# Kernel tuning notes

Measured on AMD Instinct MI355X. Metric: run time of the kernel, lower is better.

Reference implementation:

```python
import jax, jax.numpy as jnp
import numpy as np

N = 131072      # octree nodes at this depth
C_IN = 256      # in_channels == out_channels
C_B = 64        # bottleneck channels = out_channels // 4
K = 27          # 3x3x3 octree kernel neighborhood
EPS = 1e-5


def _bn(x, g, b, m, v):
    # inference-style BatchNorm with given running stats
    return (x - m) * (g * jax.lax.rsqrt(v + EPS)) + b


def setup_inputs() -> dict:
    key = jax.random.key(0)
    ks = jax.random.split(key, 20)
    inp = {
        "data": jax.random.normal(ks[0], (N, C_IN), dtype=jnp.float32),
        "neigh": jax.random.randint(ks[1], (N, K), 0, N, dtype=jnp.int32),
        "depth": 6,
        # conv1x1a (Linear, no bias) + BN
        "w1": jax.random.normal(ks[2], (C_IN, C_B), dtype=jnp.float32) * 0.05,
        "bn1_g": jax.random.uniform(ks[3], (C_B,), dtype=jnp.float32) + 0.5,
        "bn1_b": jax.random.normal(ks[4], (C_B,), dtype=jnp.float32) * 0.1,
        "bn1_m": jax.random.normal(ks[5], (C_B,), dtype=jnp.float32) * 0.1,
        "bn1_v": jax.random.uniform(ks[6], (C_B,), dtype=jnp.float32) + 0.5,
        # octree conv3x3 (27-neighbor gather + GEMM, no bias) + BN
        "w3": jax.random.normal(ks[7], (K, C_B, C_B), dtype=jnp.float32) * 0.02,
        "bn2_g": jax.random.uniform(ks[8], (C_B,), dtype=jnp.float32) + 0.5,
        "bn2_b": jax.random.normal(ks[9], (C_B,), dtype=jnp.float32) * 0.1,
        "bn2_m": jax.random.normal(ks[10], (C_B,), dtype=jnp.float32) * 0.1,
        "bn2_v": jax.random.uniform(ks[11], (C_B,), dtype=jnp.float32) + 0.5,
        # conv1x1b + BN (no ReLU)
        "w2": jax.random.normal(ks[12], (C_B, C_IN), dtype=jnp.float32) * 0.05,
        "bn3_g": jax.random.uniform(ks[13], (C_IN,), dtype=jnp.float32) + 0.5,
        "bn3_b": jax.random.normal(ks[14], (C_IN,), dtype=jnp.float32) * 0.1,
        "bn3_m": jax.random.normal(ks[15], (C_IN,), dtype=jnp.float32) * 0.1,
        "bn3_v": jax.random.uniform(ks[16], (C_IN,), dtype=jnp.float32) + 0.5,
    }
    return inp


def reference(data, neigh, depth, w1, bn1_g, bn1_b, bn1_m, bn1_v,
              w3, bn2_g, bn2_b, bn2_m, bn2_v,
              w2, bn3_g, bn3_b, bn3_m, bn3_v):
    # conv1x1a + BN + ReLU
    c1 = jax.nn.relu(_bn(data @ w1, bn1_g, bn1_b, bn1_m, bn1_v))  # [N, C_B]
    # octree conv3x3: gather 27 neighbors then contract with [K, C_B, C_B]
    gathered = c1[neigh]                                          # [N, K, C_B]
    c2 = jnp.einsum('nkc,kcd->nd', gathered, w3)                  # [N, C_B]
    c2 = jax.nn.relu(_bn(c2, bn2_g, bn2_b, bn2_m, bn2_v))
    # conv1x1b + BN (no relu)
    c3 = _bn(c2 @ w2, bn3_g, bn3_b, bn3_m, bn3_v)                 # [N, C_IN]
    # residual (in_channels == out_channels -> identity shortcut) + ReLU
    return jax.nn.relu(c3 + data)
```

## Files before the change

kernel.cpp:

```cpp
#include <hip/hip_runtime.h>

#define CIN 256
#define CB 64
#define KNB 27

typedef __attribute__((ext_vector_type(8))) short short8_t;
typedef __attribute__((ext_vector_type(4))) float f32x4;
typedef __attribute__((ext_vector_type(4))) int   i32x4;

__device__ inline unsigned short f2bf(float f) {
    union { float f; unsigned u; } x; x.f = f;
    unsigned r = x.u + 0x7fffu + ((x.u >> 16) & 1u);
    return (unsigned short)(r >> 16);
}
__device__ inline float bf2f(unsigned short h) {
    union { unsigned u; float f; } x; x.u = ((unsigned)h) << 16; return x.f;
}
__device__ inline f32x4 mfma16(short8_t a, short8_t b, f32x4 c) {
    return __builtin_amdgcn_mfma_f32_16x16x32_bf16(a, b, c, 0, 0, 0);
}
__device__ inline i32x4 mfma_i8(i32x4 a, i32x4 b, i32x4 c) {
    return __builtin_amdgcn_mfma_i32_16x16x64_i8(a, b, c, 0, 0, 0);
}

__global__ __launch_bounds__(64) void zero_kernel(unsigned* __restrict__ amax) {
    if (threadIdx.x < 4) amax[threadIdx.x] = 0u;
}

__global__ __launch_bounds__(256) void prep_a_kernel(
    const float* __restrict__ w1, const float* __restrict__ w2,
    const float* __restrict__ g1, const float* __restrict__ b1, const float* __restrict__ m1, const float* __restrict__ v1,
    const float* __restrict__ g2, const float* __restrict__ b2, const float* __restrict__ m2, const float* __restrict__ v2,
    const float* __restrict__ g3, const float* __restrict__ b3, const float* __restrict__ m3, const float* __restrict__ v3,
    unsigned short* __restrict__ w1p, unsigned short* __restrict__ w2p,
    float* __restrict__ bias1, float* __restrict__ bias2, float* __restrict__ bias3)
{
    int t = blockIdx.x * 256 + threadIdx.x;
    if (t < 16384) {
        int j = t & 7, lane = (t >> 3) & 63, tt = (t >> 9) & 3, s = t >> 11;
        int c = s * 32 + (lane >> 4) * 8 + j;
        int d = tt * 16 + (lane & 15);
        float sc = g1[d] * rsqrtf(v1[d] + 1e-5f);
        w1p[t] = f2bf(w1[c * CB + d] * sc);
    } else if (t < 32768) {
        int u = t - 16384;
        int j = u & 7, lane = (u >> 3) & 63, mt = (u >> 9) & 15, s = u >> 13;
        int c = s * 32 + (lane >> 4) * 8 + j;
        int d = mt * 16 + (lane & 15);
        float sc = g3[d] * rsqrtf(v3[d] + 1e-5f);
        w2p[u] = f2bf(w2[c * CIN + d] * sc);
    } else if (t < 33152) {
        int u = t - 32768;
        if (u < 64)       { float sc = g1[u] * rsqrtf(v1[u] + 1e-5f); bias1[u] = b1[u] - m1[u] * sc; }
        else if (u < 128) { int d = u - 64;  float sc = g2[d] * rsqrtf(v2[d] + 1e-5f); bias2[d] = b2[d] - m2[d] * sc; }
        else              { int d = u - 128; float sc = g3[d] * rsqrtf(v3[d] + 1e-5f); bias3[d] = b3[d] - m3[d] * sc; }
    }
}

__global__ __launch_bounds__(1024) void w3max_kernel(
    const float* __restrict__ w3, const float* __restrict__ g2, const float* __restrict__ v2,
    unsigned* __restrict__ amax)
{
    __shared__ float sm[16];
    int tid = threadIdx.x;
    float m = 0.f;
    for (int e = blockIdx.x * 1024 + tid; e < KNB * CB * CB; e += 8 * 1024) {
        int d = e & 63;
        float sc = g2[d] * rsqrtf(v2[d] + 1e-5f);
        m = fmaxf(m, fabsf(w3[e] * sc));
    }
#pragma unroll
    for (int off = 32; off; off >>= 1) m = fmaxf(m, __shfl_xor(m, off));
    if ((tid & 63) == 0) sm[tid >> 6] = m;
    __syncthreads();
    if (tid == 0) {
        float r = sm[0];
#pragma unroll
        for (int i = 1; i < 16; i++) r = fmaxf(r, sm[i]);
        atomicMax(&amax[1], __float_as_uint(r));
    }
}

__global__ __launch_bounds__(256) void prep_b_kernel(
    const float* __restrict__ w3, const float* __restrict__ g2, const float* __restrict__ v2,
    const unsigned* __restrict__ amax, signed char* __restrict__ w3q)
{
    int u = blockIdx.x * 256 + threadIdx.x;
    int j = u & 15, lane = (u >> 4) & 63, tile = (u >> 10) & 3, k = u >> 12;
    int c = (lane >> 4) * 16 + j;
    int d = tile * 16 + (lane & 15);
    float sw = __uint_as_float(amax[1]);
    float inv = sw > 0.f ? 127.f / sw : 0.f;
    float sc = g2[d] * rsqrtf(v2[d] + 1e-5f);
    int q = __float2int_rn(w3[(k * CB + c) * CB + d] * sc * inv);
    q = q > 127 ? 127 : (q < -127 ? -127 : q);
    w3q[u] = (signed char)q;
}

__global__ __launch_bounds__(256) void k1_conv1x1a(
    const float* __restrict__ data, const unsigned short* __restrict__ w1p,
    const float* __restrict__ bias1, unsigned short* __restrict__ c1b,
    float* __restrict__ blockmax)
{
    __shared__ short8_t w1s[2048];
    __shared__ float smax[4];
    int tid = threadIdx.x;
    const short8_t* wsrc = (const short8_t*)w1p;
#pragma unroll
    for (int i = 0; i < 8; i++) w1s[tid + i * 256] = wsrc[tid + i * 256];

    int lane = tid & 63, wave = tid >> 6;
    int g = lane >> 4, r = lane & 15;
    int rowbase = blockIdx.x * 128 + wave * 32;
    f32x4 acc[2][4] = {};
    __syncthreads();

#pragma unroll
    for (int s = 0; s < 8; s++) {
        short8_t a[2];
#pragma unroll
        for (int sub = 0; sub < 2; sub++) {
            const float* ap = data + (size_t)(rowbase + sub * 16 + r) * CIN + s * 32 + g * 8;
            float4 f0 = *(const float4*)ap;
            float4 f1 = *(const float4*)(ap + 4);
            short8_t av;
            av[0] = (short)f2bf(f0.x); av[1] = (short)f2bf(f0.y);
            av[2] = (short)f2bf(f0.z); av[3] = (short)f2bf(f0.w);
            av[4] = (short)f2bf(f1.x); av[5] = (short)f2bf(f1.y);
            av[6] = (short)f2bf(f1.z); av[7] = (short)f2bf(f1.w);
            a[sub] = av;
        }
#pragma unroll
        for (int t = 0; t < 4; t++) {
            short8_t b = w1s[(s * 4 + t) * 64 + lane];
            acc[0][t] = mfma16(a[0], b, acc[0][t]);
            acc[1][t] = mfma16(a[1], b, acc[1][t]);
        }
    }

    float mloc = 0.f;
#pragma unroll
    for (int sub = 0; sub < 2; sub++)
#pragma unroll
        for (int t = 0; t < 4; t++) {
            int col = t * 16 + r;
            float bs = bias1[col];
#pragma unroll
            for (int i = 0; i < 4; i++) {
                int row = rowbase + sub * 16 + g * 4 + i;
                float v = fmaxf(acc[sub][t][i] + bs, 0.f);
                mloc = fmaxf(mloc, v);
                c1b[row * CB + col] = f2bf(v);
            }
        }
#pragma unroll
    for (int off = 32; off; off >>= 1) mloc = fmaxf(mloc, __shfl_xor(mloc, off));
    if (lane == 0) smax[wave] = mloc;
    __syncthreads();
    if (tid == 0)
        blockmax[blockIdx.x] = fmaxf(fmaxf(smax[0], smax[1]), fmaxf(smax[2], smax[3]));
}

__global__ __launch_bounds__(1024) void c1max_kernel(
    const float* __restrict__ blockmax, unsigned* __restrict__ amax)
{
    __shared__ float sm[16];
    int tid = threadIdx.x;
    float m = blockmax[tid];
#pragma unroll
    for (int off = 32; off; off >>= 1) m = fmaxf(m, __shfl_xor(m, off));
    if ((tid & 63) == 0) sm[tid >> 6] = m;
    __syncthreads();
    if (tid == 0) {
        float r = sm[0];
#pragma unroll
        for (int i = 1; i < 16; i++) r = fmaxf(r, sm[i]);
        amax[0] = __float_as_uint(r);
    }
}

__global__ __launch_bounds__(256) void quant_c1_kernel(
    const unsigned short* __restrict__ c1b, const unsigned* __restrict__ amax,
    signed char* __restrict__ c1q)
{
    int t = blockIdx.x * 256 + threadIdx.x;
    float s1 = __uint_as_float(amax[0]);
    float inv = s1 > 0.f ? 127.f / s1 : 0.f;
    const short8_t* src = (const short8_t*)c1b;
    short8_t v0 = src[t * 2], v1 = src[t * 2 + 1];
    int ow[4];
#pragma unroll
    for (int h = 0; h < 4; h++) {
        int w = 0;
#pragma unroll
        for (int e = 0; e < 4; e++) {
            unsigned short hv = (unsigned short)((h < 2 ? v0 : v1)[(h & 1) * 4 + e]);
            int q = __float2int_rn(bf2f(hv) * inv);
            q = q > 127 ? 127 : q;
            w |= (q & 0xff) << (e * 8);
        }
        ow[h] = w;
    }
    ((int4*)c1q)[t] = make_int4(ow[0], ow[1], ow[2], ow[3]);
}

__global__ __launch_bounds__(64, 4) void k2_conv3x3(
    const signed char* __restrict__ c1q, const int* __restrict__ neigh,
    const signed char* __restrict__ w3q, const float* __restrict__ bias2,
    const unsigned* __restrict__ amax, unsigned short* __restrict__ c2b)
{
    __shared__ int nidx[32 * KNB];
    int tid = threadIdx.x;
    int rowbase = blockIdx.x * 32;

    const int4* nsrc = (const int4*)(neigh + (size_t)rowbase * KNB);
#pragma unroll
    for (int i = 0; i < 4; i++) {
        int p = tid + i * 64;
        if (p < 216) ((int4*)nidx)[p] = nsrc[p];
    }

    int lane = tid;
    int g = lane >> 4, r = lane & 15;
    float sf = __uint_as_float(amax[0]) * __uint_as_float(amax[1]) * (1.f / (127.f * 127.f));
    __syncthreads();

    const i32x4* bq = (const i32x4*)w3q;
    i32x4 iacc[2][4] = {};

#pragma unroll
    for (int k = 0; k < KNB; k++) {
        i32x4 b0 = bq[k * 256 + lane];
        i32x4 b1 = bq[k * 256 + 64 + lane];
        i32x4 b2 = bq[k * 256 + 128 + lane];
        i32x4 b3 = bq[k * 256 + 192 + lane];
        int i0 = nidx[r * KNB + k];
        int i1 = nidx[(16 + r) * KNB + k];
        i32x4 a0 = *(const i32x4*)(c1q + (size_t)i0 * CB + g * 16);
        i32x4 a1 = *(const i32x4*)(c1q + (size_t)i1 * CB + g * 16);
        iacc[0][0] = mfma_i8(a0, b0, iacc[0][0]);
        iacc[1][0] = mfma_i8(a1, b0, iacc[1][0]);
        iacc[0][1] = mfma_i8(a0, b1, iacc[0][1]);
        iacc[1][1] = mfma_i8(a1, b1, iacc[1][1]);
        iacc[0][2] = mfma_i8(a0, b2, iacc[0][2]);
        iacc[1][2] = mfma_i8(a1, b2, iacc[1][2]);
        iacc[0][3] = mfma_i8(a0, b3, iacc[0][3]);
        iacc[1][3] = mfma_i8(a1, b3, iacc[1][3]);
    }

#pragma unroll
    for (int sub = 0; sub < 2; sub++)
#pragma unroll
        for (int t = 0; t < 4; t++) {
            int col = t * 16 + r;
            float bs = bias2[col];
#pragma unroll
            for (int i = 0; i < 4; i++) {
                int row = rowbase + sub * 16 + g * 4 + i;
                float v = fmaxf((float)iacc[sub][t][i] * sf + bs, 0.f);
                c2b[row * CB + col] = f2bf(v);
            }
        }
}

__global__ __launch_bounds__(256) void k3_conv1x1b(
    const unsigned short* __restrict__ c2b, const unsigned short* __restrict__ w2p,
    const float* __restrict__ bias3, const float* __restrict__ data,
    float* __restrict__ out)
{
    int tid = threadIdx.x;
    int lane = tid & 63, wave = tid >> 6;
    int g = lane >> 4, r = lane & 15;
    int rowbase = blockIdx.x * 64;

    const short8_t* abase = (const short8_t*)w2p;
    short8_t bfr[4][2];
#pragma unroll
    for (int sub = 0; sub < 4; sub++)
#pragma unroll
        for (int s = 0; s < 2; s++)
            bfr[sub][s] = *(const short8_t*)(c2b + (size_t)(rowbase + sub * 16 + r) * CB + s * 32 + g * 8);

    f32x4 acc2[4][4] = {};
#pragma unroll
    for (int s = 0; s < 2; s++)
#pragma unroll
        for (int mt = 0; mt < 4; mt++) {
            short8_t a = abase[(s * 16 + wave * 4 + mt) * 64 + lane];
#pragma unroll
            for (int sub = 0; sub < 4; sub++)
                acc2[sub][mt] = mfma16(a, bfr[sub][s], acc2[sub][mt]);
        }

#pragma unroll
    for (int sub = 0; sub < 4; sub++)
#pragma unroll
        for (int mt = 0; mt < 4; mt++) {
            int col0 = (wave * 4 + mt) * 16 + g * 4;
            int rowg = rowbase + sub * 16 + r;
            float4 bs = *(const float4*)(bias3 + col0);
            float4 dv = *(const float4*)(data + (size_t)rowg * CIN + col0);
            f32x4 v = acc2[sub][mt];
            float4 res;
            res.x = fmaxf(v[0] + bs.x + dv.x, 0.f);
            res.y = fmaxf(v[1] + bs.y + dv.y, 0.f);
            res.z = fmaxf(v[2] + bs.z + dv.z, 0.f);
            res.w = fmaxf(v[3] + bs.w + dv.w, 0.f);
            *(float4*)(out + (size_t)rowg * CIN + col0) = res;
        }
}

extern "C" void kernel_launch(void* const* d_in, const int* in_sizes, int n_in,
                              void* d_out, int out_size, void* d_ws, size_t ws_size,
                              hipStream_t stream)
{
    const float* data = (const float*)d_in[0];
    const int* neigh  = (const int*)d_in[1];
    const float* w1 = (const float*)d_in[3];
    const float* g1 = (const float*)d_in[4];
    const float* b1 = (const float*)d_in[5];
    const float* m1 = (const float*)d_in[6];
    const float* v1 = (const float*)d_in[7];
    const float* w3 = (const float*)d_in[8];
    const float* g2 = (const float*)d_in[9];
    const float* b2 = (const float*)d_in[10];
    const float* m2 = (const float*)d_in[11];
    const float* v2 = (const float*)d_in[12];
    const float* w2 = (const float*)d_in[13];
    const float* g3 = (const float*)d_in[14];
    const float* b3 = (const float*)d_in[15];
    const float* m3 = (const float*)d_in[16];
    const float* v3 = (const float*)d_in[17];
    float* out = (float*)d_out;

    char* ws = (char*)d_ws;
    unsigned short* c1b = (unsigned short*)ws;
    unsigned short* c2b = (unsigned short*)ws;
    signed char*    c1q = (signed char*)(ws + 16777216);
    unsigned short* w1p = (unsigned short*)(ws + 25165824);
    signed char*    w3q = (signed char*)(ws + 25198592);
    unsigned short* w2p = (unsigned short*)(ws + 25309184);
    float* bias1 = (float*)(ws + 25341952);
    float* bias2 = bias1 + 64;
    float* bias3 = bias1 + 128;
    unsigned* amax = (unsigned*)(ws + 25343488);
    float* blockmax = (float*)(ws + 25343552);

    int n = in_sizes[0] / CIN;

    hipLaunchKernelGGL(zero_kernel, dim3(1), dim3(64), 0, stream, amax);
    hipLaunchKernelGGL(prep_a_kernel, dim3(130), dim3(256), 0, stream,
                       w1, w2, g1, b1, m1, v1, g2, b2, m2, v2, g3, b3, m3, v3,
                       w1p, w2p, bias1, bias2, bias3);
    hipLaunchKernelGGL(w3max_kernel, dim3(8), dim3(1024), 0, stream, w3, g2, v2, amax);
    hipLaunchKernelGGL(prep_b_kernel, dim3(432), dim3(256), 0, stream,
                       w3, g2, v2, amax, w3q);
    hipLaunchKernelGGL(k1_conv1x1a, dim3(n / 128), dim3(256), 0, stream,
                       data, w1p, bias1, c1b, blockmax);
    hipLaunchKernelGGL(c1max_kernel, dim3(1), dim3(1024), 0, stream, blockmax, amax);
    hipLaunchKernelGGL(quant_c1_kernel, dim3(2048), dim3(256), 0, stream,
                       c1b, amax, c1q);
    hipLaunchKernelGGL(k2_conv3x3, dim3(n / 32), dim3(64), 0, stream,
                       c1q, neigh, w3q, bias2, amax, c2b);
    hipLaunchKernelGGL(k3_conv1x1b, dim3(n / 64), dim3(256), 0, stream,
                       c2b, w2p, bias3, data, out);
}
```

Before: 168.7 us.

## Fuse conv3x3 with conv1x1b and fold max reductions into consumer kernels

The 27-neighbour int8 conv3x3 and the second 1x1 conv are merged into one kernel, with the bf16 intermediate staged in LDS instead of written to and re-read from global memory. The separate w3 max, w3 quantisation, c1 max and zero kernels are folded in: every block redundantly recomputes the global max before quantising. This cuts four launches and a global round trip for c2. In exchange the fused kernel has lower occupancy (launch bounds 64,3), each 64-thread block does all 256 output columns, and the w3 max is recomputed by all 432 blocks.

```diff
diff --git a/kernel.cpp b/kernel.cpp
--- a/kernel.cpp
+++ b/kernel.cpp
@@ -21,10 +21,6 @@
 }
 __device__ inline i32x4 mfma_i8(i32x4 a, i32x4 b, i32x4 c) {
     return __builtin_amdgcn_mfma_i32_16x16x64_i8(a, b, c, 0, 0, 0);
-}
-
-__global__ __launch_bounds__(64) void zero_kernel(unsigned* __restrict__ amax) {
-    if (threadIdx.x < 4) amax[threadIdx.x] = 0u;
 }
 
 __global__ __launch_bounds__(256) void prep_a_kernel(
@@ -57,44 +53,41 @@
     }
 }
 
-__global__ __launch_bounds__(1024) void w3max_kernel(
+__global__ __launch_bounds__(256) void prep_bq_kernel(
     const float* __restrict__ w3, const float* __restrict__ g2, const float* __restrict__ v2,
-    unsigned* __restrict__ amax)
-{
-    __shared__ float sm[16];
+    signed char* __restrict__ w3q, unsigned* __restrict__ amax)
+{
+    __shared__ float sc2[64];
+    __shared__ float sm[4];
     int tid = threadIdx.x;
+    if (tid < 64) sc2[tid] = g2[tid] * rsqrtf(v2[tid] + 1e-5f);
+    __syncthreads();
+
+    const float4* w34 = (const float4*)w3;
     float m = 0.f;
-    for (int e = blockIdx.x * 1024 + tid; e < KNB * CB * CB; e += 8 * 1024) {
-        int d = e & 63;
-        float sc = g2[d] * rsqrtf(v2[d] + 1e-5f);
-        m = fmaxf(m, fabsf(w3[e] * sc));
+    for (int e = tid; e < KNB * CB * CB / 4; e += 256) {
+        float4 v = w34[e];
+        int d0 = (e * 4) & 63;
+        m = fmaxf(m, fabsf(v.x * sc2[d0]));
+        m = fmaxf(m, fabsf(v.y * sc2[d0 + 1]));
+        m = fmaxf(m, fabsf(v.z * sc2[d0 + 2]));
+        m = fmaxf(m, fabsf(v.w * sc2[d0 + 3]));
     }
 #pragma unroll
     for (int off = 32; off; off >>= 1) m = fmaxf(m, __shfl_xor(m, off));
     if ((tid & 63) == 0) sm[tid >> 6] = m;
     __syncthreads();
-    if (tid == 0) {
-        float r = sm[0];
-#pragma unroll
-        for (int i = 1; i < 16; i++) r = fmaxf(r, sm[i]);
-        atomicMax(&amax[1], __float_as_uint(r));
-    }
-}
-
-__global__ __launch_bounds__(256) void prep_b_kernel(
-    const float* __restrict__ w3, const float* __restrict__ g2, const float* __restrict__ v2,
-    const unsigned* __restrict__ amax, signed char* __restrict__ w3q)
-{
-    int u = blockIdx.x * 256 + threadIdx.x;
+    float mm = fmaxf(fmaxf(sm[0], sm[1]), fmaxf(sm[2], sm[3]));
+    float inv = mm > 0.f ? 127.f / mm : 0.f;
+
+    int u = blockIdx.x * 256 + tid;
     int j = u & 15, lane = (u >> 4) & 63, tile = (u >> 10) & 3, k = u >> 12;
     int c = (lane >> 4) * 16 + j;
     int d = tile * 16 + (lane & 15);
-    float sw = __uint_as_float(amax[1]);
-    float inv = sw > 0.f ? 127.f / sw : 0.f;
-    float sc = g2[d] * rsqrtf(v2[d] + 1e-5f);
-    int q = __float2int_rn(w3[(k * CB + c) * CB + d] * sc * inv);
+    int q = __float2int_rn(w3[(k * CB + c) * CB + d] * sc2[d] * inv);
     q = q > 127 ? 127 : (q < -127 ? -127 : q);
     w3q[u] = (signed char)q;
+    if (blockIdx.x == 0 && tid == 0) amax[1] = __float_as_uint(mm);
 }
 
 __global__ __launch_bounds__(256) void k1_conv1x1a(
@@ -161,31 +154,22 @@
         blockmax[blockIdx.x] = fmaxf(fmaxf(smax[0], smax[1]), fmaxf(smax[2], smax[3]));
 }
 
-__global__ __launch_bounds__(1024) void c1max_kernel(
-    const float* __restrict__ blockmax, unsigned* __restrict__ amax)
-{
-    __shared__ float sm[16];
+__global__ __launch_bounds__(256) void quant_c1_kernel(
+    const unsigned short* __restrict__ c1b, const float* __restrict__ blockmax,
+    signed char* __restrict__ c1q, unsigned* __restrict__ amax)
+{
+    __shared__ float sm[4];
     int tid = threadIdx.x;
-    float m = blockmax[tid];
+    float4 bm = ((const float4*)blockmax)[tid];
+    float m = fmaxf(fmaxf(bm.x, bm.y), fmaxf(bm.z, bm.w));
 #pragma unroll
     for (int off = 32; off; off >>= 1) m = fmaxf(m, __shfl_xor(m, off));
     if ((tid & 63) == 0) sm[tid >> 6] = m;
     __syncthreads();
-    if (tid == 0) {
-        float r = sm[0];
-#pragma unroll
-        for (int i = 1; i < 16; i++) r = fmaxf(r, sm[i]);
-        amax[0] = __float_as_uint(r);
-    }
-}
-
-__global__ __launch_bounds__(256) void quant_c1_kernel(
-    const unsigned short* __restrict__ c1b, const unsigned* __restrict__ amax,
-    signed char* __restrict__ c1q)
-{
-    int t = blockIdx.x * 256 + threadIdx.x;
-    float s1 = __uint_as_float(amax[0]);
+    float s1 = fmaxf(fmaxf(sm[0], sm[1]), fmaxf(sm[2], sm[3]));
     float inv = s1 > 0.f ? 127.f / s1 : 0.f;
+
+    int t = blockIdx.x * 256 + tid;
     const short8_t* src = (const short8_t*)c1b;
     short8_t v0 = src[t * 2], v1 = src[t * 2 + 1];
     int ow[4];
@@ -202,14 +186,18 @@
         ow[h] = w;
     }
     ((int4*)c1q)[t] = make_int4(ow[0], ow[1], ow[2], ow[3]);
-}
-
-__global__ __launch_bounds__(64, 4) void k2_conv3x3(
+    if (blockIdx.x == 0 && tid == 0) amax[0] = __float_as_uint(s1);
+}
+
+__global__ __launch_bounds__(64, 3) void k23_fused(
     const signed char* __restrict__ c1q, const int* __restrict__ neigh,
     const signed char* __restrict__ w3q, const float* __restrict__ bias2,
-    const unsigned* __restrict__ amax, unsigned short* __restrict__ c2b)
+    const unsigned* __restrict__ amax,
+    const unsigned short* __restrict__ w2p, const float* __restrict__ bias3,
+    const float* __restrict__ data, float* __restrict__ out)
 {
     __shared__ int nidx[32 * KNB];
+    __shared__ unsigned short cst[32 * 68];
     int tid = threadIdx.x;
     int rowbase = blockIdx.x * 32;
 
@@ -220,20 +208,18 @@
         if (p < 216) ((int4*)nidx)[p] = nsrc[p];
     }
 
-    int lane = tid;
-    int g = lane >> 4, r = lane & 15;
+    int g = tid >> 4, r = tid & 15;
     float sf = __uint_as_float(amax[0]) * __uint_as_float(amax[1]) * (1.f / (127.f * 127.f));
     __syncthreads();
 
     const i32x4* bq = (const i32x4*)w3q;
     i32x4 iacc[2][4] = {};
-
 #pragma unroll
     for (int k = 0; k < KNB; k++) {
-        i32x4 b0 = bq[k * 256 + lane];
-        i32x4 b1 = bq[k * 256 + 64 + lane];
-        i32x4 b2 = bq[k * 256 + 128 + lane];
-        i32x4 b3 = bq[k * 256 + 192 + lane];
+        i32x4 b0 = bq[k * 256 + tid];
+        i32x4 b1 = bq[k * 256 + 64 + tid];
+        i32x4 b2 = bq[k * 256 + 128 + tid];
+        i32x4 b3 = bq[k * 256 + 192 + tid];
         int i0 = nidx[r * KNB + k];
         int i1 = nidx[(16 + r) * KNB + k];
         i32x4 a0 = *(const i32x4*)(c1q + (size_t)i0 * CB + g * 16);
@@ -256,58 +242,49 @@
             float bs = bias2[col];
 #pragma unroll
             for (int i = 0; i < 4; i++) {
-                int row = rowbase + sub * 16 + g * 4 + i;
-                float v = fmaxf((float)iacc[sub][t][i] * sf + bs, 0.f);
-                c2b[row * CB + col] = f2bf(v);
+                int lrow = sub * 16 + g * 4 + i;
+                cst[lrow * 68 + col] = f2bf(fmaxf((float)iacc[sub][t][i] * sf + bs, 0.f));
             }
         }
-}
-
-__global__ __launch_bounds__(256) void k3_conv1x1b(
-    const unsigned short* __restrict__ c2b, const unsigned short* __restrict__ w2p,
-    const float* __restrict__ bias3, const float* __restrict__ data,
-    float* __restrict__ out)
-{
-    int tid = threadIdx.x;
-    int lane = tid & 63, wave = tid >> 6;
-    int g = lane >> 4, r = lane & 15;
-    int rowbase = blockIdx.x * 64;
+    __syncthreads();
+
+    short8_t bfr[2][2];
+#pragma unroll
+    for (int sub = 0; sub < 2; sub++)
+#pragma unroll
+        for (int s = 0; s < 2; s++)
+            bfr[sub][s] = *(const short8_t*)&cst[(sub * 16 + r) * 68 + s * 32 + g * 8];
 
     const short8_t* abase = (const short8_t*)w2p;
-    short8_t bfr[4][2];
-#pragma unroll
-    for (int sub = 0; sub < 4; sub++)
-#pragma unroll
-        for (int s = 0; s < 2; s++)
-            bfr[sub][s] = *(const short8_t*)(c2b + (size_t)(rowbase + sub * 16 + r) * CB + s * 32 + g * 8);
-
-    f32x4 acc2[4][4] = {};
-#pragma unroll
-    for (int s = 0; s < 2; s++)
-#pragma unroll
-        for (int mt = 0; mt < 4; mt++) {
-            short8_t a = abase[(s * 16 + wave * 4 + mt) * 64 + lane];
-#pragma unroll
-            for (int sub = 0; sub < 4; sub++)
-                acc2[sub][mt] = mfma16(a, bfr[sub][s], acc2[sub][mt]);
-        }
-
-#pragma unroll
-    for (int sub = 0; sub < 4; sub++)
-#pragma unroll
-        for (int mt = 0; mt < 4; mt++) {
-            int col0 = (wave * 4 + mt) * 16 + g * 4;
-            int rowg = rowbase + sub * 16 + r;
-            float4 bs = *(const float4*)(bias3 + col0);
-            float4 dv = *(const float4*)(data + (size_t)rowg * CIN + col0);
-            f32x4 v = acc2[sub][mt];
-            float4 res;
-            res.x = fmaxf(v[0] + bs.x + dv.x, 0.f);
-            res.y = fmaxf(v[1] + bs.y + dv.y, 0.f);
-            res.z = fmaxf(v[2] + bs.z + dv.z, 0.f);
-            res.w = fmaxf(v[3] + bs.w + dv.w, 0.f);
-            *(float4*)(out + (size_t)rowg * CIN + col0) = res;
-        }
+#pragma unroll
+    for (int h = 0; h < 2; h++) {
+        f32x4 acc2[2][8] = {};
+#pragma unroll
+        for (int mt = 0; mt < 8; mt++) {
+            short8_t a0 = abase[(h * 8 + mt) * 64 + tid];
+            short8_t a1 = abase[(16 + h * 8 + mt) * 64 + tid];
+            acc2[0][mt] = mfma16(a0, bfr[0][0], acc2[0][mt]);
+            acc2[0][mt] = mfma16(a1, bfr[0][1], acc2[0][mt]);
+            acc2[1][mt] = mfma16(a0, bfr[1][0], acc2[1][mt]);
+            acc2[1][mt] = mfma16(a1, bfr[1][1], acc2[1][mt]);
+        }
+#pragma unroll
+        for (int sub = 0; sub < 2; sub++)
+#pragma unroll
+            for (int mt = 0; mt < 8; mt++) {
+                int col0 = (h * 8 + mt) * 16 + g * 4;
+                int rowg = rowbase + sub * 16 + r;
+                float4 bs = *(const float4*)(bias3 + col0);
+                float4 dv = *(const float4*)(data + (size_t)rowg * CIN + col0);
+                f32x4 v = acc2[sub][mt];
+                float4 res;
+                res.x = fmaxf(v[0] + bs.x + dv.x, 0.f);
+                res.y = fmaxf(v[1] + bs.y + dv.y, 0.f);
+                res.z = fmaxf(v[2] + bs.z + dv.z, 0.f);
+                res.w = fmaxf(v[3] + bs.w + dv.w, 0.f);
+                *(float4*)(out + (size_t)rowg * CIN + col0) = res;
+            }
+    }
 }
 
 extern "C" void kernel_launch(void* const* d_in, const int* in_sizes, int n_in,
@@ -335,7 +312,6 @@
 
     char* ws = (char*)d_ws;
     unsigned short* c1b = (unsigned short*)ws;
-    unsigned short* c2b = (unsigned short*)ws;
     signed char*    c1q = (signed char*)(ws + 16777216);
     unsigned short* w1p = (unsigned short*)(ws + 25165824);
     signed char*    w3q = (signed char*)(ws + 25198592);
@@ -348,20 +324,15 @@
 
     int n = in_sizes[0] / CIN;
 
-    hipLaunchKernelGGL(zero_kernel, dim3(1), dim3(64), 0, stream, amax);
     hipLaunchKernelGGL(prep_a_kernel, dim3(130), dim3(256), 0, stream,
                        w1, w2, g1, b1, m1, v1, g2, b2, m2, v2, g3, b3, m3, v3,
                        w1p, w2p, bias1, bias2, bias3);
-    hipLaunchKernelGGL(w3max_kernel, dim3(8), dim3(1024), 0, stream, w3, g2, v2, amax);
-    hipLaunchKernelGGL(prep_b_kernel, dim3(432), dim3(256), 0, stream,
-                       w3, g2, v2, amax, w3q);
+    hipLaunchKernelGGL(prep_bq_kernel, dim3(432), dim3(256), 0, stream,
+                       w3, g2, v2, w3q, amax);
     hipLaunchKernelGGL(k1_conv1x1a, dim3(n / 128), dim3(256), 0, stream,
                        data, w1p, bias1, c1b, blockmax);
-    hipLaunchKernelGGL(c1max_kernel, dim3(1), dim3(1024), 0, stream, blockmax, amax);
     hipLaunchKernelGGL(quant_c1_kernel, dim3(2048), dim3(256), 0, stream,
-                       c1b, amax, c1q);
-    hipLaunchKernelGGL(k2_conv3x3, dim3(n / 32), dim3(64), 0, stream,
-                       c1q, neigh, w3q, bias2, amax, c2b);
-    hipLaunchKernelGGL(k3_conv1x1b, dim3(n / 64), dim3(256), 0, stream,
-                       c2b, w2p, bias3, data, out);
-}
+                       c1b, blockmax, c1q, amax);
+    hipLaunchKernelGGL(k23_fused, dim3(n / 32), dim3(64), 0, stream,
+                       c1q, neigh, w3q, bias2, amax, w2p, bias3, data, out);
+}
```

Result: slower. 186.9 us (+10.8%).
